# Kernel optimization log

Hardware: AMD Instinct MI355X
Metric: run time of the kernel (lower is better)

The kernel has to match this reference:

```python
import jax, jax.numpy as jnp
import numpy as np

B, N, D = 4, 1024, 1024
H, KV, HD = 16, 4, 64
S, CTX = 128, 2048
MLPD = 4096
NITER, DT = 2, 0.1


def _rms(x, w, eps=1e-6):
    return x * jax.lax.rsqrt(jnp.mean(x * x, axis=-1, keepdims=True) + eps) * w


def _gelu(x):
    return jax.nn.gelu(x, approximate=False)  # torch nn.GELU() is exact erf


def _rope(q, k, cos, sin):
    # q: [B,H,N,HD], cos/sin: [N, HD//2]; interleaved-half RoPE as in source
    q1, q2 = q[..., ::2], q[..., 1::2]
    k1, k2 = k[..., ::2], k[..., 1::2]
    c = cos[None, None]
    s = sin[None, None]
    q_rot = jnp.concatenate([q1 * c - q2 * s, q1 * s + q2 * c], axis=-1)
    k_rot = jnp.concatenate([k1 * c - k2 * s, k1 * s + k2 * c], axis=-1)
    return q_rot, k_rot


def setup_inputs():
    key = jax.random.key(0)
    ks = jax.random.split(key, 24)
    rn = lambda k, shp, s=0.02: jax.random.normal(k, shp, jnp.float32) * s
    inv = 1.0 / (10000.0 ** (jnp.arange(0, HD, 2, dtype=jnp.float32) / HD))  # [HD//2]
    ang = jnp.arange(N, dtype=jnp.float32)[:, None] * inv[None, :]
    return {
        'x': jax.random.normal(ks[0], (B, N, D), jnp.float32),
        'c': jax.random.normal(ks[1], (B, D), jnp.float32),
        'context': jax.random.normal(ks[2], (B, S, CTX), jnp.float32),
        'cos': jnp.cos(ang), 'sin': jnp.sin(ang),
        'wq': rn(ks[3], (D, D)), 'wk': rn(ks[4], (D, KV * HD)),
        'wv': rn(ks[5], (D, KV * HD)), 'wo': rn(ks[6], (D, D)),
        'cwq': rn(ks[7], (D, D)), 'cwk': rn(ks[8], (CTX, D)),
        'cwv': rn(ks[9], (CTX, D)), 'cwo': rn(ks[10], (D, D)),
        'fc1_w': rn(ks[11], (D, MLPD)), 'fc1_b': jnp.zeros((MLPD,), jnp.float32),
        'fc2_w': rn(ks[12], (MLPD, D)), 'fc2_b': jnp.zeros((D,), jnp.float32),
        'ada_w': rn(ks[13], (D, 6 * D)), 'ada_b': jnp.zeros((6 * D,), jnp.float32),
        'n1': jnp.ones((D,), jnp.float32), 'n2': jnp.ones((D,), jnp.float32), 'n3': jnp.ones((D,), jnp.float32),
        'int_w': jnp.full((D,), 0.5, jnp.float32), 'mu': jnp.zeros((D,), jnp.float32),
        'hg1_w': rn(ks[14], (D, D // 4)), 'hg1_b': jnp.zeros((D // 4,), jnp.float32),
        'hg2_w': rn(ks[15], (D // 4, 1)), 'hg2_b': jnp.zeros((1,), jnp.float32),
        'ct1_w': rn(ks[16], (2 * D, D // 2)), 'ct1_b': jnp.zeros((D // 2,), jnp.float32),
        'ct2_w': rn(ks[17], (D // 2, 3 * D)), 'ct2_b': jnp.zeros((3 * D,), jnp.float32),
        'rf1_w': rn(ks[18], (D, 2 * D)), 'rf1_b': jnp.zeros((2 * D,), jnp.float32),
        'rf2_w': rn(ks[19], (2 * D, D)), 'rf2_b': jnp.zeros((D,), jnp.float32),
    }


def _forward(x, c, context, cos, sin, wq, wk, wv, wo, cwq, cwk, cwv, cwo,
             fc1_w, fc1_b, fc2_w, fc2_b, ada_w, ada_b, n1, n2, n3, int_w, mu,
             hg1_w, hg1_b, hg2_w, hg2_b, ct1_w, ct1_b, ct2_w, ct2_b,
             rf1_w, rf1_b, rf2_w, rf2_b):
    scale = HD ** -0.5
    # AdaLN-Zero modulation from timestep conditioning c: [B, 6D]
    mod = jax.nn.silu(c) @ ada_w + ada_b
    sh_msa, sc_msa, g_msa, sh_mlp, sc_mlp, g_mlp = jnp.split(mod, 6, axis=-1)
    # --- GQA self-attention with RoPE ---
    h = _rms(x, n1) * (1.0 + sc_msa[:, None, :]) + sh_msa[:, None, :]
    q = (h @ wq).reshape(B, N, H, HD).transpose(0, 2, 1, 3)
    k = (h @ wk).reshape(B, N, KV, HD).transpose(0, 2, 1, 3)
    v = (h @ wv).reshape(B, N, KV, HD).transpose(0, 2, 1, 3)
    q, k = _rope(q, k, cos, sin)
    k = jnp.repeat(k, H // KV, axis=1)  # repeat_interleave over head dim
    v = jnp.repeat(v, H // KV, axis=1)
    attn = jax.nn.softmax(jnp.einsum('bhnd,bhmd->bhnm', q, k) * scale, axis=-1)
    sa = jnp.einsum('bhnm,bhmd->bhnd', attn, v).transpose(0, 2, 1, 3).reshape(B, N, D) @ wo
    x = x + g_msa[:, None, :] * sa
    # --- cross-attention (text conditioning) ---
    h2 = _rms(x, n2)
    qc = (h2 @ cwq).reshape(B, N, H, HD).transpose(0, 2, 1, 3)
    kc = (context @ cwk).reshape(B, S, H, HD).transpose(0, 2, 1, 3)
    vc = (context @ cwv).reshape(B, S, H, HD).transpose(0, 2, 1, 3)
    ca = jax.nn.softmax(jnp.einsum('bhnd,bhsd->bhns', qc, kc) * scale, axis=-1)
    xa = jnp.einsum('bhns,bhsd->bhnd', ca, vc).transpose(0, 2, 1, 3).reshape(B, N, D) @ cwo
    x = x + xa
    # --- AdaLN-modulated MLP ---
    h3 = _rms(x, n3) * (1.0 + sc_mlp[:, None, :]) + sh_mlp[:, None, :]
    m = _gelu(h3 @ fc1_w + fc1_b) @ fc2_w + fc2_b
    x = x + g_mlp[:, None, :] * m
    # --- IntegratorNeuron: damped-oscillator halting dynamics ---
    vst = jnp.zeros_like(x)
    integ = x
    halt_probs = []
    for _ in range(NITER):
        ctrl = _gelu(jnp.concatenate([integ, vst], axis=-1) @ ct1_w + ct1_b) @ ct2_w + ct2_b
        a_raw, b_raw, g_raw = jnp.split(ctrl, 3, axis=-1)
        alpha = jax.nn.sigmoid(a_raw)
        beta = jax.nn.softplus(b_raw)
        gate = jax.nn.sigmoid(g_raw)
        v_next = alpha * vst - beta * (integ - mu)
        x_next = integ + DT * gate * v_next
        hp = jax.nn.sigmoid(_gelu(x_next @ hg1_w + hg1_b) @ hg2_w + hg2_b)  # [B,N,1]
        refined = _gelu(x_next @ rf1_w + rf1_b) @ rf2_w + rf2_b
        integ = integ + hp * refined * int_w
        vst = v_next
        halt_probs.append(hp)
    return integ, jnp.stack(halt_probs, axis=1)


def reference(x, c, context, cos, sin, wq, wk, wv, wo, cwq, cwk, cwv, cwo,
              fc1_w, fc1_b, fc2_w, fc2_b, ada_w, ada_b, n1, n2, n3, int_w, mu,
              hg1_w, hg1_b, hg2_w, hg2_b, ct1_w, ct1_b, ct2_w, ct2_b,
              rf1_w, rf1_b, rf2_w, rf2_b):
    return _forward(x, c, context, cos, sin, wq, wk, wv, wo, cwq, cwk, cwv, cwo,
                    fc1_w, fc1_b, fc2_w, fc2_b, ada_w, ada_b, n1, n2, n3, int_w, mu,
                    hg1_w, hg1_b, hg2_w, hg2_b, ct1_w, ct1_b, ct2_w, ct2_b,
                    rf1_w, rf1_b, rf2_w, rf2_b)
```

## Files before the change

kernel.cpp:

```cpp
#include <hip/hip_runtime.h>
#include <hip/hip_bf16.h>
#include <math.h>

typedef __hip_bfloat16 bf16;
typedef unsigned short ushort;
typedef __bf16 bf16x8 __attribute__((ext_vector_type(8)));
typedef unsigned short u16x8 __attribute__((ext_vector_type(8)));
typedef float f32x4 __attribute__((ext_vector_type(4)));

#define BB 4
#define NN 1024
#define DD 1024
#define HH 16
#define KVH 4
#define HDIM 64
#define SS 128
#define CTXD 2048
#define MLPDIM 4096

__device__ __forceinline__ float bf2f(bf16 v){ return __bfloat162float(v); }
__device__ __forceinline__ bf16 f2bf(float v){ return __float2bfloat16(v); }
__device__ __forceinline__ ushort fbits(float v){ bf16 h = __float2bfloat16(v); return *(ushort*)&h; }
__device__ __forceinline__ float ubf(ushort u){ unsigned int x = ((unsigned int)u) << 16; float f; *(unsigned int*)&f = x; return f; }
__device__ __forceinline__ float sigmf_(float x){ return 1.f/(1.f+expf(-x)); }
__device__ __forceinline__ float geluf_(float x){ return 0.5f*x*(1.f+erff(x*0.70710678118f)); }

typedef const __attribute__((address_space(1))) void* gas_t;
typedef __attribute__((address_space(3))) void* las_t;
__device__ __forceinline__ void gl2lds16(const void* g, void* l){
  __builtin_amdgcn_global_load_lds((gas_t)g, (las_t)l, 16, 0, 0);
}

__device__ __forceinline__ int xcd_swz_flat(int flat, int total){
  return (flat & 7)*(total >> 3) + (flat >> 3);
}

__global__ void k_copy4(const float4* __restrict__ in, float4* __restrict__ out, int n4){
  int i = blockIdx.x*256 + threadIdx.x;
  if (i < n4) out[i] = in[i];
}
__global__ void k_f2bfv(const float* __restrict__ in, bf16* __restrict__ out, int n){
  int i = blockIdx.x*256 + threadIdx.x;
  if (i < n) out[i] = f2bf(in[i]);
}
__global__ void k_silu(const float* __restrict__ c, float* __restrict__ out, int n){
  int i = blockIdx.x*256 + threadIdx.x;
  if (i < n){ float v = c[i]; out[i] = v*sigmf_(v); }
}
__global__ void k_zero16(unsigned short* __restrict__ p, int n){
  int i = blockIdx.x*256 + threadIdx.x;
  if (i < n) p[i] = 0;
}

__global__ __launch_bounds__(256) void k_wt(const float* __restrict__ in, bf16* __restrict__ out, int K, int N){
  __shared__ float t[64][65];
  int bn = blockIdx.x*64, bk = blockIdx.y*64;
  int tid = threadIdx.x;
  int c4 = (tid & 15)*4, r = tid >> 4;
  #pragma unroll
  for (int i = 0; i < 4; ++i){
    float4 v = *(const float4*)(in + (size_t)(bk + r + i*16)*N + bn + c4);
    t[c4+0][r+i*16] = v.x; t[c4+1][r+i*16] = v.y; t[c4+2][r+i*16] = v.z; t[c4+3][r+i*16] = v.w;
  }
  __syncthreads();
  int n = tid >> 2, k16 = (tid & 3)*16;
  bf16* orow = out + (size_t)(bn + n)*K + bk + k16;
  #pragma unroll
  for (int j = 0; j < 16; ++j) orow[j] = f2bf(t[n][k16 + j]);
}

__global__ void k_adab(const float* __restrict__ b, float* __restrict__ mod, int n){
  int idx = blockIdx.x*256 + threadIdx.x;
  if (idx < n) mod[idx] = b[idx % 6144];
}
__global__ __launch_bounds__(256) void k_ada2(const float* __restrict__ sc, const float* __restrict__ w,
                       float* __restrict__ mod){
  __shared__ float sl[4][32];
  int tid = threadIdx.x;
  int col4 = blockIdx.x*1024 + tid*4;
  int k0 = blockIdx.y*32;
  if (tid < 128) sl[tid >> 5][tid & 31] = sc[(tid >> 5)*DD + k0 + (tid & 31)];
  __syncthreads();
  f32x4 acc[4] = {};
  for (int kk = 0; kk < 32; ++kk){
    const float4 wv4 = *(const float4*)(w + (size_t)(k0 + kk)*6144 + col4);
    #pragma unroll
    for (int b = 0; b < 4; ++b){
      float s = sl[b][kk];
      acc[b][0] += s*wv4.x; acc[b][1] += s*wv4.y; acc[b][2] += s*wv4.z; acc[b][3] += s*wv4.w;
    }
  }
  #pragma unroll
  for (int b = 0; b < 4; ++b)
    #pragma unroll
    for (int j = 0; j < 4; ++j)
      atomicAdd(&mod[(size_t)b*6144 + col4 + j], acc[b][j]);
}

__global__ __launch_bounds__(256) void k_rms(const float* __restrict__ X, const float* __restrict__ w,
                      const float* __restrict__ mod, int sc_off, int sh_off,
                      bf16* __restrict__ out, int use_mod){
  __shared__ float red[256];
  int row = blockIdx.x;
  int b = row >> 10;
  int tid = threadIdx.x;
  const float* xr = X + (size_t)row*DD;
  float s = 0.f;
  #pragma unroll
  for (int i = 0; i < 4; ++i){ float v = xr[tid + i*256]; s += v*v; }
  red[tid] = s; __syncthreads();
  for (int st = 128; st > 0; st >>= 1){ if (tid < st) red[tid] += red[tid+st]; __syncthreads(); }
  float rstd = rsqrtf(red[0]*(1.f/DD) + 1e-6f);
  bf16* orow = out + (size_t)row*DD;
  const float* mrow = use_mod ? (mod + (size_t)b*6*DD) : nullptr;
  #pragma unroll
  for (int i = 0; i < 4; ++i){
    int d = tid + i*256;
    float v = xr[d]*rstd*w[d];
    if (use_mod) v = v*(1.f + mrow[sc_off + d]) + mrow[sh_off + d];
    orow[d] = f2bf(v);
  }
}

__global__ __launch_bounds__(256,2) void k_mm2(const ushort* __restrict__ A, const ushort* __restrict__ BT,
                      const float* __restrict__ bias, ushort* __restrict__ C,
                      int M, int N, int K, int act){
  __shared__ ushort As[128*64];
  __shared__ ushort Bs[128*64];
  int tid = threadIdx.x, lane = tid & 63, wv = tid >> 6;
  int l15 = lane & 15, quad = lane >> 4;
  int gx = gridDim.x;
  int nf = xcd_swz_flat(blockIdx.y*gx + blockIdx.x, gx*gridDim.y);
  int bm = (nf / gx)*128, bn = (nf % gx)*128;
  int wm = (wv & 1)*64, wn = (wv >> 1)*64;
  int lr = lane >> 3, lc = lane & 7;
  int ksw = (lc ^ lr) << 3;
  f32x4 acc[4][4] = {};
  const ushort* Abase = A  + (size_t)(bm + wv*32 + lr)*K + ksw;
  const ushort* Bbase = BT + (size_t)(bn + wv*32 + lr)*K + ksw;
  ushort* AsW = As + wv*2048;
  ushort* BsW = Bs + wv*2048;
  int swr = (l15 & 7) << 3;
  for (int k0 = 0; k0 < K; k0 += 64){
    #pragma unroll
    for (int i = 0; i < 4; ++i){
      gl2lds16(Abase + k0 + (size_t)(i*8)*K, AsW + i*512);
      gl2lds16(Bbase + k0 + (size_t)(i*8)*K, BsW + i*512);
    }
    __syncthreads();
    #pragma unroll
    for (int ks = 0; ks < 2; ++ks){
      bf16x8 af[4], bfr[4];
      #pragma unroll
      for (int mi = 0; mi < 4; ++mi){
        int r = wm + mi*16 + l15;
        af[mi] = __builtin_bit_cast(bf16x8, *(const uint4*)(As + r*64 + ((ks*32 + quad*8) ^ swr)));
      }
      #pragma unroll
      for (int nj = 0; nj < 4; ++nj){
        int r = wn + nj*16 + l15;
        bfr[nj] = __builtin_bit_cast(bf16x8, *(const uint4*)(Bs + r*64 + ((ks*32 + quad*8) ^ swr)));
      }
      #pragma unroll
      for (int mi = 0; mi < 4; ++mi)
        #pragma unroll
        for (int nj = 0; nj < 4; ++nj)
          acc[mi][nj] = __builtin_amdgcn_mfma_f32_16x16x32_bf16(af[mi], bfr[nj], acc[mi][nj], 0, 0, 0);
    }
    __syncthreads();
  }
  #pragma unroll
  for (int nj = 0; nj < 4; ++nj){
    int col = bn + wn + nj*16 + l15;
    float bv = bias ? bias[col] : 0.f;
    #pragma unroll
    for (int mi = 0; mi < 4; ++mi){
      #pragma unroll
      for (int r = 0; r < 4; ++r){
        int row = bm + wm + mi*16 + quad*4 + r;
        float v = acc[mi][nj][r] + bv;
        if (act) v = geluf_(v);
        C[(size_t)row*N + col] = fbits(v);
      }
    }
  }
}

__global__ __launch_bounds__(256,2) void k_mm2h(const ushort* __restrict__ A, const ushort* __restrict__ BT,
                      const float* __restrict__ bias, ushort* __restrict__ C,
                      int M, int N, int K, int act){
  __shared__ ushort As[128*64];
  __shared__ ushort Bs[64*64];
  int tid = threadIdx.x, lane = tid & 63, wv = tid >> 6;
  int l15 = lane & 15, quad = lane >> 4;
  int gx = gridDim.x;
  int nf = xcd_swz_flat(blockIdx.y*gx + blockIdx.x, gx*gridDim.y);
  int bm = (nf / gx)*128, bn = (nf % gx)*64;
  int wm = wv*32;
  int lr = lane >> 3, lc = lane & 7;
  int ksw = (lc ^ lr) << 3;
  f32x4 acc[2][4] = {};
  const ushort* Abase = A  + (size_t)(bm + wv*32 + lr)*K + ksw;
  const ushort* Bbase = BT + (size_t)(bn + wv*16 + lr)*K + ksw;
  ushort* AsW = As + wv*2048;
  ushort* BsW = Bs + wv*1024;
  int swr = (l15 & 7) << 3;
  for (int k0 = 0; k0 < K; k0 += 64){
    #pragma unroll
    for (int i = 0; i < 4; ++i)
      gl2lds16(Abase + k0 + (size_t)(i*8)*K, AsW + i*512);
    #pragma unroll
    for (int i = 0; i < 2; ++i)
      gl2lds16(Bbase + k0 + (size_t)(i*8)*K, BsW + i*512);
    __syncthreads();
    #pragma unroll
    for (int ks = 0; ks < 2; ++ks){
      bf16x8 af[2], bfr[4];
      #pragma unroll
      for (int mi = 0; mi < 2; ++mi){
        int r = wm + mi*16 + l15;
        af[mi] = __builtin_bit_cast(bf16x8, *(const uint4*)(As + r*64 + ((ks*32 + quad*8) ^ swr)));
      }
      #pragma unroll
      for (int nj = 0; nj < 4; ++nj){
        int r = nj*16 + l15;
        bfr[nj] = __builtin_bit_cast(bf16x8, *(const uint4*)(Bs + r*64 + ((ks*32 + quad*8) ^ swr)));
      }
      #pragma unroll
      for (int mi = 0; mi < 2; ++mi)
        #pragma unroll
        for (int nj = 0; nj < 4; ++nj)
          acc[mi][nj] = __builtin_amdgcn_mfma_f32_16x16x32_bf16(af[mi], bfr[nj], acc[mi][nj], 0, 0, 0);
    }
    __syncthreads();
  }
  #pragma unroll
  for (int nj = 0; nj < 4; ++nj){
    int col = bn + nj*16 + l15;
    float bv = bias ? bias[col] : 0.f;
    #pragma unroll
    for (int mi = 0; mi < 2; ++mi){
      #pragma unroll
      for (int r = 0; r < 4; ++r){
        int row = bm + wm + mi*16 + quad*4 + r;
        float v = acc[mi][nj][r] + bv;
        if (act) v = geluf_(v);
        C[(size_t)row*N + col] = fbits(v);
      }
    }
  }
}

__global__ void k_rope(const bf16* __restrict__ in, const float* __restrict__ cw,
                       const float* __restrict__ sw, bf16* __restrict__ out, int NHp, int n){
  int idx = blockIdx.x*256 + threadIdx.x;
  if (idx >= n) return;
  int d2 = idx & 31; int t = idx >> 5;
  int nn = t % NN; t /= NN; int h = t % NHp; int b = t / NHp;
  const bf16* base = in + ((size_t)((b*NN+nn)*NHp + h))*HDIM;
  float e = bf2f(base[2*d2]), o = bf2f(base[2*d2+1]);
  float c = cw[nn*32 + d2], s = sw[nn*32 + d2];
  bf16* ob = out + ((size_t)((b*NHp+h)*NN + nn))*HDIM;
  ob[d2]      = f2bf(e*c - o*s);
  ob[32 + d2] = f2bf(e*s + o*c);
}

__global__ void k_tr(const bf16* __restrict__ in, bf16* __restrict__ out, int T, int NHp, int n){
  int idx = blockIdx.x*256 + threadIdx.x;
  if (idx >= n) return;
  int d = idx & 63; int t = idx >> 6;
  int h = t % NHp; t /= NHp; int tok = t % T; int b = t / T;
  out[((size_t)((b*NHp+h)*T + tok))*64 + d] = in[idx];
}

__global__ void k_trv(const bf16* __restrict__ in, bf16* __restrict__ out, int T, int NHp, int n){
  int idx = blockIdx.x*256 + threadIdx.x;
  if (idx >= n) return;
  int d = idx & 63; int t = idx >> 6;
  int h = t % NHp; t /= NHp; int tok = t % T; int b = t / T;
  out[((size_t)(b*NHp+h)*64 + d)*T + tok] = in[idx];
}

__global__ __launch_bounds__(256) void k_fattn(const ushort* __restrict__ Q, const ushort* __restrict__ K,
                      const ushort* __restrict__ V, ushort* __restrict__ O,
                      int NH, int NKV, int Nq, int Nk, float scale){
  __shared__ ushort Kt[64*64];
  __shared__ ushort Vt[64*64];
  __shared__ ushort Ps[4][16*72];
  int tid = threadIdx.x, lane = tid & 63, wv = tid >> 6;
  int l15 = lane & 15, quad = lane >> 4;
  int lr = lane >> 3, lc = lane & 7;
  int ksw = (lc ^ lr) << 3;
  int swr = (l15 & 7) << 3;
  int nqt = Nq >> 6;
  int nf = xcd_swz_flat(blockIdx.x, gridDim.x);
  int qt = nf % nqt; int t = nf / nqt; int h = t % NH; int b = t / NH;
  int kvh = h / (NH / NKV);
  const ushort* Kb = K + (size_t)(b*NKV+kvh)*Nk*64 + ksw;
  const ushort* Vb = V + (size_t)(b*NKV+kvh)*64*Nk + ksw;
  const ushort* Qp = Q + ((size_t)((b*NH+h)*Nq + qt*64 + wv*16 + l15))*64;
  float qscale = scale * 1.44269504f;
  uint4 qraw0 = *(const uint4*)(Qp + quad*8);
  uint4 qraw1 = *(const uint4*)(Qp + 32 + quad*8);
  u16x8 q0 = __builtin_bit_cast(u16x8, qraw0), q1 = __builtin_bit_cast(u16x8, qraw1);
  #pragma unroll
  for (int j = 0; j < 8; ++j){ q0[j] = fbits(ubf(q0[j])*qscale); q1[j] = fbits(ubf(q1[j])*qscale); }
  bf16x8 qf0 = __builtin_bit_cast(bf16x8, q0);
  bf16x8 qf1 = __builtin_bit_cast(bf16x8, q1);
  f32x4 acc[4] = {};
  float m_run[4]  = {0.f,0.f,0.f,0.f};
  float l_part[4] = {0.f,0.f,0.f,0.f};
  ushort* Pw = Ps[wv];
  int wrow = wv*16;
  for (int t0 = 0; t0 < Nk; t0 += 64){
    #pragma unroll
    for (int i = 0; i < 2; ++i){
      int row = wrow + i*8 + lr;
      gl2lds16(Kb + (size_t)(t0+row)*64, Kt + (wrow + i*8)*64);
      gl2lds16(Vb + (size_t)row*Nk + t0, Vt + (wrow + i*8)*64);
    }
    __syncthreads();
    f32x4 s[4] = {};
    __builtin_amdgcn_s_setprio(1);
    #pragma unroll
    for (int nj = 0; nj < 4; ++nj){
      const ushort* kr = Kt + (nj*16+l15)*64;
      bf16x8 kf0 = __builtin_bit_cast(bf16x8, *(const uint4*)(kr + ((quad*8) ^ swr)));
      s[nj] = __builtin_amdgcn_mfma_f32_16x16x32_bf16(qf0, kf0, s[nj], 0, 0, 0);
      bf16x8 kf1 = __builtin_bit_cast(bf16x8, *(const uint4*)(kr + ((32 + quad*8) ^ swr)));
      s[nj] = __builtin_amdgcn_mfma_f32_16x16x32_bf16(qf1, kf1, s[nj], 0, 0, 0);
    }
    __builtin_amdgcn_s_setprio(0);
    float tl[4];
    #pragma unroll
    for (int r = 0; r < 4; ++r)
      tl[r] = fmaxf(fmaxf(s[0][r], s[1][r]), fmaxf(s[2][r], s[3][r]));
    float dmax = fmaxf(fmaxf(tl[0]-m_run[0], tl[1]-m_run[1]),
                       fmaxf(tl[2]-m_run[2], tl[3]-m_run[3]));
    if (__any(dmax > 8.f)){
      #pragma unroll
      for (int r = 0; r < 4; ++r){
        float tm = tl[r];
        #pragma unroll
        for (int off = 8; off; off >>= 1) tm = fmaxf(tm, __shfl_xor(tm, off, 64));
        float mn = fmaxf(m_run[r], tm);
        float al = exp2f(m_run[r] - mn);
        m_run[r] = mn;
        l_part[r] *= al;
        #pragma unroll
        for (int nj = 0; nj < 4; ++nj) acc[nj][r] *= al;
      }
    }
    #pragma unroll
    for (int nj = 0; nj < 4; ++nj)
      #pragma unroll
      for (int r = 0; r < 4; ++r){
        float p = exp2f(s[nj][r] - m_run[r]);
        s[nj][r] = p;
        Pw[(quad*4+r)*72 + nj*16 + l15] = fbits(p);
      }
    #pragma unroll
    for (int r = 0; r < 4; ++r)
      l_part[r] += (s[0][r]+s[1][r]) + (s[2][r]+s[3][r]);
    bf16x8 pf0 = __builtin_bit_cast(bf16x8, *(const uint4*)(Pw + l15*72 + quad*8));
    bf16x8 pf1 = __builtin_bit_cast(bf16x8, *(const uint4*)(Pw + l15*72 + 32 + quad*8));
    __builtin_amdgcn_s_setprio(1);
    #pragma unroll
    for (int nj = 0; nj < 4; ++nj){
      const ushort* vr = Vt + (nj*16+l15)*64;
      bf16x8 vf0 = __builtin_bit_cast(bf16x8, *(const uint4*)(vr + ((quad*8) ^ swr)));
      acc[nj] = __builtin_amdgcn_mfma_f32_16x16x32_bf16(pf0, vf0, acc[nj], 0, 0, 0);
      bf16x8 vf1 = __builtin_bit_cast(bf16x8, *(const uint4*)(vr + ((32 + quad*8) ^ swr)));
      acc[nj] = __builtin_amdgcn_mfma_f32_16x16x32_bf16(pf1, vf1, acc[nj], 0, 0, 0);
    }
    __builtin_amdgcn_s_setprio(0);
    __syncthreads();
  }
  float inv[4];
  #pragma unroll
  for (int r = 0; r < 4; ++r){
    float ls = l_part[r];
    #pragma unroll
    for (int off = 8; off; off >>= 1) ls += __shfl_xor(ls, off, 64);
    inv[r] = 1.f / ls;
  }
  int nbase = qt*64 + wv*16 + quad*4;
  #pragma unroll
  for (int r = 0; r < 4; ++r){
    size_t ob = ((size_t)((b*Nq + nbase + r)*NH + h))*64;
    #pragma unroll
    for (int nj = 0; nj < 4; ++nj)
      O[ob + nj*16 + l15] = fbits(acc[nj][r]*inv[r]);
  }
}

__global__ void k_resid(float* __restrict__ X, const float* __restrict__ base,
                        const bf16* __restrict__ val,
                        const float* __restrict__ mod, int goff, int n){
  int i = blockIdx.x*256 + threadIdx.x;
  if (i >= n) return;
  float g = 1.f;
  if (mod){ int b = i >> 20; int d = i & 1023; g = mod[b*6144 + goff + d]; }
  float x0 = base ? base[i] : X[i];
  X[i] = x0 + g*bf2f(val[i]);
}

__global__ void k_concat(const float* __restrict__ X, const bf16* __restrict__ V,
                         bf16* __restrict__ C, int n){
  int i = blockIdx.x*256 + threadIdx.x;
  if (i >= n) return;
  int row = i >> 11, col = i & 2047;
  C[i] = (col < 1024) ? f2bf(X[(size_t)row*1024 + col]) : V[(size_t)row*1024 + col - 1024];
}

__global__ void k_ctrl(const bf16* __restrict__ ctrl, const float* __restrict__ X,
                       bf16* __restrict__ VST, bf16* __restrict__ XN,
                       const float* __restrict__ mu, int n){
  int i = blockIdx.x*256 + threadIdx.x;
  if (i >= n) return;
  int row = i >> 10, d = i & 1023;
  const bf16* cr = ctrl + (size_t)row*3072;
  float alpha = sigmf_(bf2f(cr[d]));
  float braw  = bf2f(cr[1024 + d]);
  float beta  = fmaxf(braw, 0.f) + log1pf(expf(-fabsf(braw)));
  float gate  = sigmf_(bf2f(cr[2048 + d]));
  float vn = alpha*bf2f(VST[i]) - beta*(X[i] - mu[d]);
  VST[i] = f2bf(vn);
  XN[i]  = f2bf(X[i] + 0.1f*gate*vn);
}

__global__ __launch_bounds__(64) void k_hg2(const bf16* __restrict__ hin, const float* __restrict__ w,
                     const float* __restrict__ bb, float* __restrict__ hp,
                     float* __restrict__ oout, int it){
  int r = blockIdx.x; int lane = threadIdx.x;
  const bf16* hr = hin + (size_t)r*256;
  float s = 0.f;
  #pragma unroll
  for (int i = 0; i < 4; ++i) s += bf2f(hr[lane + i*64])*w[lane + i*64];
  for (int off = 32; off; off >>= 1) s += __shfl_xor(s, off, 64);
  if (lane == 0){
    float v = sigmf_(s + bb[0]);
    hp[r] = v;
    int b = r >> 10, nn = r & 1023;
    oout[((size_t)(b*2 + it) << 10) + nn] = v;
  }
}

__global__ void k_integ(float* __restrict__ X, const float* __restrict__ hp,
                        const bf16* __restrict__ rf, const float* __restrict__ iw, int n){
  int i = blockIdx.x*256 + threadIdx.x;
  if (i >= n) return;
  int row = i >> 10, d = i & 1023;
  X[i] += hp[row]*bf2f(rf[i])*iw[d];
}

extern "C" void kernel_launch(void* const* d_in, const int* in_sizes, int n_in,
                              void* d_out, int out_size, void* d_ws, size_t ws_size,
                              hipStream_t stream) {
  const float* x_in  = (const float*)d_in[0];
  const float* c_in  = (const float*)d_in[1];
  const float* ctx_in= (const float*)d_in[2];
  const float* cosw  = (const float*)d_in[3];
  const float* sinw  = (const float*)d_in[4];
  const float* wq    = (const float*)d_in[5];
  const float* wk    = (const float*)d_in[6];
  const float* wv    = (const float*)d_in[7];
  const float* wo    = (const float*)d_in[8];
  const float* cwq   = (const float*)d_in[9];
  const float* cwk   = (const float*)d_in[10];
  const float* cwv   = (const float*)d_in[11];
  const float* cwo   = (const float*)d_in[12];
  const float* fc1_w = (const float*)d_in[13];
  const float* fc1_b = (const float*)d_in[14];
  const float* fc2_w = (const float*)d_in[15];
  const float* fc2_b = (const float*)d_in[16];
  const float* ada_w = (const float*)d_in[17];
  const float* ada_b = (const float*)d_in[18];
  const float* n1    = (const float*)d_in[19];
  const float* n2    = (const float*)d_in[20];
  const float* n3    = (const float*)d_in[21];
  const float* int_w = (const float*)d_in[22];
  const float* mu    = (const float*)d_in[23];
  const float* hg1_w = (const float*)d_in[24];
  const float* hg1_b = (const float*)d_in[25];
  const float* hg2_w = (const float*)d_in[26];
  const float* hg2_b = (const float*)d_in[27];
  const float* ct1_w = (const float*)d_in[28];
  const float* ct1_b = (const float*)d_in[29];
  const float* ct2_w = (const float*)d_in[30];
  const float* ct2_b = (const float*)d_in[31];
  const float* rf1_w = (const float*)d_in[32];
  const float* rf1_b = (const float*)d_in[33];
  const float* rf2_w = (const float*)d_in[34];
  const float* rf2_b = (const float*)d_in[35];

  float* out_f  = (float*)d_out;
  float* out_hp = out_f + (size_t)BB*NN*DD;

  char* wsb = (char*)d_ws;
  const size_t Mi = 1u << 20;
  float* X  = (float*)wsb;
  bf16*  Hh = (bf16*)(wsb + 16*Mi);
  bf16*  Qb = (bf16*)(wsb + 24*Mi);
  bf16*  R  = (bf16*)(wsb + 32*Mi);
  bf16*  QR  = R;
  bf16*  SAb = R + 4*Mi;
  bf16*  KP  = R + 8*Mi;
  bf16*  VP  = R + 9*Mi;
  bf16*  KR  = R + 10*Mi;
  bf16*  VR  = R + 11*Mi;
  bf16*  CTXB= R + 12*Mi;
  bf16*  BIG = R;
  bf16*  CT1 = R + 12*Mi;
  bf16*  HG1 = R + 12*Mi;
  bf16*  RFO = R + 8*Mi;
  float* SIL = (float*)(wsb + 64*Mi);
  float* MOD = SIL + 4096;
  float* HP  = MOD + 24576;
  bf16*  VST = Qb;
  bf16*  XN  = Hh;
  bf16* WT   = (bf16*)(wsb + 65*Mi);
  bf16* wqT  = WT;
  bf16* wkT  = wqT  + 1048576;
  bf16* wvT  = wkT  + 262144;
  bf16* woT  = wvT  + 262144;
  bf16* cwqT = woT  + 1048576;
  bf16* cwkT = cwqT + 1048576;
  bf16* cwvT = cwkT + 2097152;
  bf16* cwoT = cwvT + 2097152;
  bf16* fc1T = cwoT + 1048576;
  bf16* fc2T = fc1T + 4194304;
  bf16* ct1T = fc2T + 4194304;
  bf16* ct2T = ct1T + 1048576;
  bf16* rf1T = ct2T + 1572864;
  bf16* rf2T = rf1T + 2097152;
  bf16* hg1T = rf2T + 2097152;

  const int NT = BB*NN*DD;
  const float scale = 0.125f;
  #define G1(n) dim3(((n)+255)/256), dim3(256)
  #define WTR(src,dst,K,N) k_wt<<<dim3((N)/64,(K)/64), dim3(256), 0, stream>>>((src),(dst),(K),(N))
  #define MM(Aptr,BTptr,biasptr,Cptr,M,N,K,act) \
    k_mm2<<<dim3((N)/128,(M)/128), dim3(256), 0, stream>>>((const ushort*)(Aptr),(const ushort*)(BTptr),(biasptr),(ushort*)(Cptr),(M),(N),(K),(act))
  #define MMH(Aptr,BTptr,biasptr,Cptr,M,N,K,act) \
    k_mm2h<<<dim3((N)/64,(M)/128), dim3(256), 0, stream>>>((const ushort*)(Aptr),(const ushort*)(BTptr),(biasptr),(ushort*)(Cptr),(M),(N),(K),(act))

  WTR(wq,   wqT, 1024, 1024);
  WTR(wk,   wkT, 1024, 256);
  WTR(wv,   wvT, 1024, 256);
  WTR(wo,   woT, 1024, 1024);
  WTR(cwq,  cwqT,1024, 1024);
  WTR(cwk,  cwkT,2048, 1024);
  WTR(cwv,  cwvT,2048, 1024);
  WTR(cwo,  cwoT,1024, 1024);
  WTR(fc1_w,fc1T,1024, 4096);
  WTR(fc2_w,fc2T,4096, 1024);
  WTR(ct1_w,ct1T,2048, 512);
  WTR(ct2_w,ct2T,512,  3072);
  WTR(rf1_w,rf1T,1024, 2048);
  WTR(rf2_w,rf2T,2048, 1024);
  WTR(hg1_w,hg1T,1024, 256);

  k_silu<<<G1(BB*DD), 0, stream>>>(c_in, SIL, BB*DD);
  k_adab<<<G1(BB*6144), 0, stream>>>(ada_b, MOD, BB*6144);
  k_ada2<<<dim3(6,32), dim3(256), 0, stream>>>(SIL, ada_w, MOD);

  k_rms<<<dim3(4096), dim3(256), 0, stream>>>(x_in, n1, MOD, DD, 0, Hh, 1);
  MM(Hh, wqT, nullptr, Qb, 4096, 1024, 1024, 0);
  MMH(Hh, wkT, nullptr, KP, 4096, 256, 1024, 0);
  MMH(Hh, wvT, nullptr, VP, 4096, 256, 1024, 0);
  k_rope<<<G1(BB*HH*NN*32), 0, stream>>>(Qb, cosw, sinw, QR, HH, BB*HH*NN*32);
  k_rope<<<G1(BB*KVH*NN*32), 0, stream>>>(KP, cosw, sinw, KR, KVH, BB*KVH*NN*32);
  k_trv<<<G1(BB*NN*KVH*64), 0, stream>>>(VP, VR, NN, KVH, BB*NN*KVH*64);
  k_fattn<<<dim3(BB*HH*(NN/64)), dim3(256), 0, stream>>>((const ushort*)QR, (const ushort*)KR,
      (const ushort*)VR, (ushort*)SAb, HH, KVH, NN, NN, scale);
  MM(SAb, woT, nullptr, Hh, 4096, 1024, 1024, 0);
  k_resid<<<G1(NT), 0, stream>>>(X, x_in, Hh, MOD, 2*DD, NT);

  k_rms<<<dim3(4096), dim3(256), 0, stream>>>(X, n2, nullptr, 0, 0, Hh, 0);
  MM(Hh, cwqT, nullptr, Qb, 4096, 1024, 1024, 0);
  k_tr<<<G1(NT), 0, stream>>>(Qb, QR, NN, HH, NT);
  k_f2bfv<<<G1(BB*SS*CTXD), 0, stream>>>(ctx_in, CTXB, BB*SS*CTXD);
  MMH(CTXB, cwkT, nullptr, KP, 512, 1024, 2048, 0);
  MMH(CTXB, cwvT, nullptr, VP, 512, 1024, 2048, 0);
  k_tr<<<G1(BB*SS*HH*64), 0, stream>>>(KP, KR, SS, HH, BB*SS*HH*64);
  k_trv<<<G1(BB*SS*HH*64), 0, stream>>>(VP, VR, SS, HH, BB*SS*HH*64);
  k_fattn<<<dim3(BB*HH*(NN/64)), dim3(256), 0, stream>>>((const ushort*)QR, (const ushort*)KR,
      (const ushort*)VR, (ushort*)SAb, HH, HH, NN, SS, scale);
  MM(SAb, cwoT, nullptr, Hh, 4096, 1024, 1024, 0);
  k_resid<<<G1(NT), 0, stream>>>(X, nullptr, Hh, nullptr, 0, NT);

  k_rms<<<dim3(4096), dim3(256), 0, stream>>>(X, n3, MOD, 4*DD, 3*DD, Hh, 1);
  MM(Hh, fc1T, fc1_b, BIG, 4096, 4096, 1024, 1);
  MMH(BIG, fc2T, fc2_b, Qb, 4096, 1024, 4096, 0);
  k_resid<<<G1(NT), 0, stream>>>(X, nullptr, Qb, MOD, 5*DD, NT);

  k_zero16<<<G1(NT), 0, stream>>>((unsigned short*)VST, NT);
  for (int it = 0; it < 2; ++it){
    k_concat<<<G1(2*NT), 0, stream>>>(X, VST, BIG, 2*NT);
    MMH(BIG, ct1T, ct1_b, CT1, 4096, 512, 2048, 1);
    MM(CT1, ct2T, ct2_b, BIG, 4096, 3072, 512, 0);
    k_ctrl<<<G1(NT), 0, stream>>>(BIG, X, VST, XN, mu, NT);
    MMH(XN, hg1T, hg1_b, HG1, 4096, 256, 1024, 1);
    k_hg2<<<dim3(4096), dim3(64), 0, stream>>>(HG1, hg2_w, hg2_b, HP, out_hp, it);
    MM(XN, rf1T, rf1_b, BIG, 4096, 2048, 1024, 1);
    MMH(BIG, rf2T, rf2_b, RFO, 4096, 1024, 2048, 0);
    k_integ<<<G1(NT), 0, stream>>>(X, HP, RFO, int_w, NT);
  }
  k_copy4<<<G1(NT/4), 0, stream>>>((const float4*)X, (float4*)out_f, NT/4);
  #undef G1
  #undef WTR
  #undef MM
  #undef MMH
}
```

Measured before the change: 1.044 ms.

## Double-buffer LDS tiles in GEMM kernels to overlap loads with MFMA

Both GEMM kernels (k_mm2 and k_mm2h) now use two LDS buffers. The next K-tile is issued with direct global-to-LDS loads while MFMAs run on the current tile, and the per-iteration barrier pair becomes a single waitcnt plus barrier. The goal is to hide global memory latency behind compute. LDS use doubles to 64KB and 48KB per block, which may reduce how many blocks fit per CU under launch_bounds(256,2). There is also a possible hazard: a wave may issue the next stage's writes into a buffer that slower waves are still reading, since only one barrier guards each iteration.

```diff
diff --git a/kernel.cpp b/kernel.cpp
--- a/kernel.cpp
+++ b/kernel.cpp
@@ -125,8 +125,8 @@
 __global__ __launch_bounds__(256,2) void k_mm2(const ushort* __restrict__ A, const ushort* __restrict__ BT,
                       const float* __restrict__ bias, ushort* __restrict__ C,
                       int M, int N, int K, int act){
-  __shared__ ushort As[128*64];
-  __shared__ ushort Bs[128*64];
+  __shared__ ushort As[2*128*64];
+  __shared__ ushort Bs[2*128*64];
   int tid = threadIdx.x, lane = tid & 63, wv = tid >> 6;
   int l15 = lane & 15, quad = lane >> 4;
   int gx = gridDim.x;
@@ -138,28 +138,32 @@
   f32x4 acc[4][4] = {};
   const ushort* Abase = A  + (size_t)(bm + wv*32 + lr)*K + ksw;
   const ushort* Bbase = BT + (size_t)(bn + wv*32 + lr)*K + ksw;
-  ushort* AsW = As + wv*2048;
-  ushort* BsW = Bs + wv*2048;
   int swr = (l15 & 7) << 3;
-  for (int k0 = 0; k0 < K; k0 += 64){
+
+  auto stage = [&](int buf, int k0){
+    ushort* AsW = As + buf*8192 + wv*2048;
+    ushort* BsW = Bs + buf*8192 + wv*2048;
     #pragma unroll
     for (int i = 0; i < 4; ++i){
       gl2lds16(Abase + k0 + (size_t)(i*8)*K, AsW + i*512);
       gl2lds16(Bbase + k0 + (size_t)(i*8)*K, BsW + i*512);
     }
-    __syncthreads();
+  };
+  auto compute = [&](int buf){
+    const ushort* Ab = As + buf*8192;
+    const ushort* Bb = Bs + buf*8192;
     #pragma unroll
     for (int ks = 0; ks < 2; ++ks){
       bf16x8 af[4], bfr[4];
       #pragma unroll
       for (int mi = 0; mi < 4; ++mi){
         int r = wm + mi*16 + l15;
-        af[mi] = __builtin_bit_cast(bf16x8, *(const uint4*)(As + r*64 + ((ks*32 + quad*8) ^ swr)));
+        af[mi] = __builtin_bit_cast(bf16x8, *(const uint4*)(Ab + r*64 + ((ks*32 + quad*8) ^ swr)));
       }
       #pragma unroll
       for (int nj = 0; nj < 4; ++nj){
         int r = wn + nj*16 + l15;
-        bfr[nj] = __builtin_bit_cast(bf16x8, *(const uint4*)(Bs + r*64 + ((ks*32 + quad*8) ^ swr)));
+        bfr[nj] = __builtin_bit_cast(bf16x8, *(const uint4*)(Bb + r*64 + ((ks*32 + quad*8) ^ swr)));
       }
       #pragma unroll
       for (int mi = 0; mi < 4; ++mi)
@@ -167,8 +171,23 @@
         for (int nj = 0; nj < 4; ++nj)
           acc[mi][nj] = __builtin_amdgcn_mfma_f32_16x16x32_bf16(af[mi], bfr[nj], acc[mi][nj], 0, 0, 0);
     }
-    __syncthreads();
-  }
+  };
+
+  stage(0, 0);
+  asm volatile("s_waitcnt vmcnt(0)" ::: "memory");
+  __builtin_amdgcn_s_barrier();
+  __builtin_amdgcn_sched_barrier(0);
+  int cur = 0;
+  for (int k0 = 64; k0 < K; k0 += 64){
+    stage(cur ^ 1, k0);
+    compute(cur);
+    asm volatile("s_waitcnt vmcnt(0)" ::: "memory");
+    __builtin_amdgcn_s_barrier();
+    __builtin_amdgcn_sched_barrier(0);
+    cur ^= 1;
+  }
+  compute(cur);
+
   #pragma unroll
   for (int nj = 0; nj < 4; ++nj){
     int col = bn + wn + nj*16 + l15;
@@ -189,8 +208,8 @@
 __global__ __launch_bounds__(256,2) void k_mm2h(const ushort* __restrict__ A, const ushort* __restrict__ BT,
                       const float* __restrict__ bias, ushort* __restrict__ C,
                       int M, int N, int K, int act){
-  __shared__ ushort As[128*64];
-  __shared__ ushort Bs[64*64];
+  __shared__ ushort As[2*128*64];
+  __shared__ ushort Bs[2*64*64];
   int tid = threadIdx.x, lane = tid & 63, wv = tid >> 6;
   int l15 = lane & 15, quad = lane >> 4;
   int gx = gridDim.x;
@@ -202,29 +221,33 @@
   f32x4 acc[2][4] = {};
   const ushort* Abase = A  + (size_t)(bm + wv*32 + lr)*K + ksw;
   const ushort* Bbase = BT + (size_t)(bn + wv*16 + lr)*K + ksw;
-  ushort* AsW = As + wv*2048;
-  ushort* BsW = Bs + wv*1024;
   int swr = (l15 & 7) << 3;
-  for (int k0 = 0; k0 < K; k0 += 64){
+
+  auto stage = [&](int buf, int k0){
+    ushort* AsW = As + buf*8192 + wv*2048;
+    ushort* BsW = Bs + buf*4096 + wv*1024;
     #pragma unroll
     for (int i = 0; i < 4; ++i)
       gl2lds16(Abase + k0 + (size_t)(i*8)*K, AsW + i*512);
     #pragma unroll
     for (int i = 0; i < 2; ++i)
       gl2lds16(Bbase + k0 + (size_t)(i*8)*K, BsW + i*512);
-    __syncthreads();
+  };
+  auto compute = [&](int buf){
+    const ushort* Ab = As + buf*8192;
+    const ushort* Bb = Bs + buf*4096;
     #pragma unroll
     for (int ks = 0; ks < 2; ++ks){
       bf16x8 af[2], bfr[4];
       #pragma unroll
       for (int mi = 0; mi < 2; ++mi){
         int r = wm + mi*16 + l15;
-        af[mi] = __builtin_bit_cast(bf16x8, *(const uint4*)(As + r*64 + ((ks*32 + quad*8) ^ swr)));
+        af[mi] = __builtin_bit_cast(bf16x8, *(const uint4*)(Ab + r*64 + ((ks*32 + quad*8) ^ swr)));
       }
       #pragma unroll
       for (int nj = 0; nj < 4; ++nj){
         int r = nj*16 + l15;
-        bfr[nj] = __builtin_bit_cast(bf16x8, *(const uint4*)(Bs + r*64 + ((ks*32 + quad*8) ^ swr)));
+        bfr[nj] = __builtin_bit_cast(bf16x8, *(const uint4*)(Bb + r*64 + ((ks*32 + quad*8) ^ swr)));
       }
       #pragma unroll
       for (int mi = 0; mi < 2; ++mi)
@@ -232,8 +255,23 @@
         for (int nj = 0; nj < 4; ++nj)
           acc[mi][nj] = __builtin_amdgcn_mfma_f32_16x16x32_bf16(af[mi], bfr[nj], acc[mi][nj], 0, 0, 0);
     }
-    __syncthreads();
-  }
+  };
+
+  stage(0, 0);
+  asm volatile("s_waitcnt vmcnt(0)" ::: "memory");
+  __builtin_amdgcn_s_barrier();
+  __builtin_amdgcn_sched_barrier(0);
+  int cur = 0;
+  for (int k0 = 64; k0 < K; k0 += 64){
+    stage(cur ^ 1, k0);
+    compute(cur);
+    asm volatile("s_waitcnt vmcnt(0)" ::: "memory");
+    __builtin_amdgcn_s_barrier();
+    __builtin_amdgcn_sched_barrier(0);
+    cur ^= 1;
+  }
+  compute(cur);
+
   #pragma unroll
   for (int nj = 0; nj < 4; ++nj){
     int col = bn + nj*16 + l15;
```

Measured after the change: 1.057 ms. No clear change (+1.2%).
